# Performance work log

Measured on AMD Instinct MI355X. Metric: run time of the kernel, lower is better.

Reference implementation:

```python
import jax, jax.numpy as jnp
import numpy as np

B, S, E, R = 128, 16, 512, 1000
_SCALE = np.float32(1.0 / np.sqrt(E))


def setup_inputs() -> dict:
    key = jax.random.key(0)
    ks = jax.random.split(key, 12)
    s = 1.0 / np.sqrt(E)
    u = lambda k, shape: jax.random.uniform(k, shape, jnp.float32, -s, s)
    emb = jax.random.normal(ks[0], (R + 1, E), jnp.float32).at[R].set(0.0)  # padding_idx row = 0
    return {
        "tokens": jax.random.randint(ks[11], (B, S), 0, R),
        "emb": emb,
        "W_ih": u(ks[1], (3 * E, E)), "W_hh": u(ks[2], (3 * E, E)),
        "b_ih": u(ks[3], (3 * E,)), "b_hh": u(ks[4], (3 * E,)),
        "w_fc": u(ks[5], (E,)), "b_fc": u(ks[6], ()),
        "Wq": u(ks[7], (E, E)), "bq": u(ks[8], (E,)),
        "Wk": u(ks[9], (E, E)), "bk": u(ks[10], (E,)),
    }


def _gru_step(x, h, W_ih, W_hh, b_ih, b_hh):
    # torch GRU cell: gates stacked as [r; z; n]
    gi = x @ W_ih.T + b_ih
    gh = h @ W_hh.T + b_hh
    ir, iz, inn = jnp.split(gi, 3, axis=-1)
    hr, hz, hn = jnp.split(gh, 3, axis=-1)
    r = jax.nn.sigmoid(ir + hr)
    z = jax.nn.sigmoid(iz + hz)
    n = jnp.tanh(inn + r * hn)
    return (1.0 - z) * n + z * h


def _attention(x, emb, Wq, bq, Wk, bk):
    # x: [B,1,E]; key = fc_k(cat(relation_emb, x)); scores = q k^T / sqrt(E)
    Bn = x.shape[0]
    rel = jnp.broadcast_to(emb[:R][None], (Bn, R, E))
    all_emb = jnp.concatenate([rel, x], axis=1)        # [B,R+1,E]
    q = x @ Wq.T + bq
    k = all_emb @ Wk.T + bk
    scores = jnp.einsum('bqe,bke->bqk', q, k) * _SCALE  # [B,1,R+1]
    return scores, all_emb


def _entropy(scores):
    lp = jax.nn.log_softmax(scores, axis=-1)
    return -jnp.sum(jnp.exp(lp) * lp, axis=-1)          # [B,1]


def _reduce(x, emb, W_ih, W_hh, b_ih, b_hh, w_fc, b_fc, Wq, bq, Wk, bk):
    Bn, L, Ed = x.shape
    if L > 2:
        # vectorized 2-step GRU over all adjacent pairs (replaces python while loop)
        h1 = _gru_step(x[:, :-1], jnp.zeros_like(x[:, :-1]), W_ih, W_hh, b_ih, b_hh)
        pairs = _gru_step(x[:, 1:], h1, W_ih, W_hh, b_ih, b_hh)   # [B,L-1,E]
        score = jax.nn.sigmoid(pairs @ w_fc + b_fc)               # [B,L-1]
        sel = jnp.argmax(score, axis=-1)                          # [B]
        barange = jnp.arange(Bn)
        pair = pairs[barange, sel][:, None]                       # [B,1,E]
        scores, all_emb = _attention(pair, emb, Wq, bq, Wk, bk)
        loss = _entropy(scores)
        prob = jax.nn.softmax(scores, axis=-1)                    # weightedAverage mask is all-False for seq_len=1
        merged = jnp.einsum('bqk,bke->bqe', prob, all_emb)[:, 0]  # [B,E]
        # output = inputs.detach().clone(); overwrite sel with merged; delete row sel+1
        out = jax.lax.stop_gradient(x).at[barange, sel].set(merged)
        j = jnp.arange(L - 1)[None]
        src = j + (j >= (sel + 1)[:, None])                       # skip zeroed row sel+1
        out = out[barange[:, None], src]                          # [B,L-1,E]
        return out, loss
    else:
        h1 = _gru_step(x[:, 0], jnp.zeros_like(x[:, 0]), W_ih, W_hh, b_ih, b_hh)
        h2 = _gru_step(x[:, 1], h1, W_ih, W_hh, b_ih, b_hh)
        return h2[:, None], jnp.zeros((Bn, 1), x.dtype)


def reference(tokens, emb, W_ih, W_hh, b_ih, b_hh, w_fc, b_fc, Wq, bq, Wk, bk):
    x = emb[tokens]                                               # [B,S,E]
    losses = []
    for _ in range(tokens.shape[1] - 1):
        x, l = _reduce(x, emb, W_ih, W_hh, b_ih, b_hh, w_fc, b_fc, Wq, bq, Wk, bk)
        losses.append(l)
    scores, _ = _attention(x, emb, Wq, bq, Wk, bk)                # x is [B,1,E]
    losses.append(_entropy(scores))
    return scores[:, 0], jnp.concatenate(losses, axis=-1)         # ([B,R+1], [B,S])
```

## Files before the change

kernel.cpp:

```cpp
#include <hip/hip_runtime.h>

#define B 128
#define S 16
#define E 512
#define R 1000
#define K3 1536
#define NW0 1920
#define NWS 256
#define NS (B * (R + 1))
#define SCALE 0.04419417382415922f

static __device__ __forceinline__ float sigm(float x) { return 1.f / (1.f + expf(-x)); }

static __device__ __forceinline__ float brsum(float v, float* sb) {
  int tid = threadIdx.x;
  sb[tid] = v; __syncthreads();
  for (int s = 128; s > 0; s >>= 1) {
    if (tid < s) sb[tid] += sb[tid + s];
    __syncthreads();
  }
  float r = sb[0]; __syncthreads();
  return r;
}
static __device__ __forceinline__ float brmax(float v, float* sb) {
  int tid = threadIdx.x;
  sb[tid] = v; __syncthreads();
  for (int s = 128; s > 0; s >>= 1) {
    if (tid < s) sb[tid] = fmaxf(sb[tid], sb[tid + s]);
    __syncthreads();
  }
  float r = sb[0]; __syncthreads();
  return r;
}
static __device__ __forceinline__ void brsum2(float v1, float v2, float* sb, float* sb2,
                                              float* o1, float* o2) {
  int tid = threadIdx.x;
  sb[tid] = v1; sb2[tid] = v2; __syncthreads();
  for (int s = 128; s > 0; s >>= 1) {
    if (tid < s) { sb[tid] += sb[tid + s]; sb2[tid] += sb2[tid + s]; }
    __syncthreads();
  }
  *o1 = sb[0]; *o2 = sb2[0]; __syncthreads();
}

#define TILE_FMA \
  _Pragma("unroll") \
  for (int k = 0; k < 16; ++k) { \
    float4 a4 = *(const float4*)&As[k][ty * 4]; \
    float4 w4 = *(const float4*)&Ws[k][tx * 4]; \
    acc[0][0] = fmaf(a4.x, w4.x, acc[0][0]); acc[0][1] = fmaf(a4.x, w4.y, acc[0][1]); \
    acc[0][2] = fmaf(a4.x, w4.z, acc[0][2]); acc[0][3] = fmaf(a4.x, w4.w, acc[0][3]); \
    acc[1][0] = fmaf(a4.y, w4.x, acc[1][0]); acc[1][1] = fmaf(a4.y, w4.y, acc[1][1]); \
    acc[1][2] = fmaf(a4.y, w4.z, acc[1][2]); acc[1][3] = fmaf(a4.y, w4.w, acc[1][3]); \
    acc[2][0] = fmaf(a4.z, w4.x, acc[2][0]); acc[2][1] = fmaf(a4.z, w4.y, acc[2][1]); \
    acc[2][2] = fmaf(a4.z, w4.z, acc[2][2]); acc[2][3] = fmaf(a4.z, w4.w, acc[2][3]); \
    acc[3][0] = fmaf(a4.w, w4.x, acc[3][0]); acc[3][1] = fmaf(a4.w, w4.y, acc[3][1]); \
    acc[3][2] = fmaf(a4.w, w4.z, acc[3][2]); acc[3][3] = fmaf(a4.w, w4.w, acc[3][3]); \
  }

#define TILE_FMA32 \
  _Pragma("unroll") \
  for (int k = 0; k < 16; ++k) { \
    float2 a2 = *(const float2*)&As[k][ty * 2]; \
    float4 w4 = *(const float4*)&Ws[k][tx * 4]; \
    acc[0][0] = fmaf(a2.x, w4.x, acc[0][0]); acc[0][1] = fmaf(a2.x, w4.y, acc[0][1]); \
    acc[0][2] = fmaf(a2.x, w4.z, acc[0][2]); acc[0][3] = fmaf(a2.x, w4.w, acc[0][3]); \
    acc[1][0] = fmaf(a2.y, w4.x, acc[1][0]); acc[1][1] = fmaf(a2.y, w4.y, acc[1][1]); \
    acc[1][2] = fmaf(a2.y, w4.z, acc[1][2]); acc[1][3] = fmaf(a2.y, w4.w, acc[1][3]); \
  }

__global__ __launch_bounds__(256) void k_gemm(const float* __restrict__ A, int lda, int M,
                                              const float* __restrict__ W, int N, int K,
                                              const float* __restrict__ bias, float scale,
                                              float* __restrict__ C, int ldc) {
  __shared__ float As[16][64];
  __shared__ float Ws[16][64];
  int tid = threadIdx.x;
  int mBase = blockIdx.y * 64;
  int nBase = blockIdx.x * 64;
  int tx = tid & 15, ty = tid >> 4;
  int li = tid & 63;
  int lk = (tid >> 6) * 4;
  float acc[4][4] = {{0.f,0.f,0.f,0.f},{0.f,0.f,0.f,0.f},{0.f,0.f,0.f,0.f},{0.f,0.f,0.f,0.f}};
  int m = mBase + li;
  const float* Arow = (m < M) ? (A + (size_t)m * lda) : nullptr;
  int n = nBase + li;
  const float* Wrow = (n < N) ? (W + (size_t)n * K) : nullptr;

  float4 av = Arow ? *(const float4*)(Arow + lk) : make_float4(0.f, 0.f, 0.f, 0.f);
  float4 wv = Wrow ? *(const float4*)(Wrow + lk) : make_float4(0.f, 0.f, 0.f, 0.f);

  for (int k0 = 0; k0 < K; k0 += 16) {
    As[lk + 0][li] = av.x; As[lk + 1][li] = av.y;
    As[lk + 2][li] = av.z; As[lk + 3][li] = av.w;
    Ws[lk + 0][li] = wv.x; Ws[lk + 1][li] = wv.y;
    Ws[lk + 2][li] = wv.z; Ws[lk + 3][li] = wv.w;
    __syncthreads();
    if (k0 + 16 < K) {
      av = Arow ? *(const float4*)(Arow + k0 + 16 + lk) : make_float4(0.f, 0.f, 0.f, 0.f);
      wv = Wrow ? *(const float4*)(Wrow + k0 + 16 + lk) : make_float4(0.f, 0.f, 0.f, 0.f);
    }
    TILE_FMA
    __syncthreads();
  }
#pragma unroll
  for (int r = 0; r < 4; ++r) {
    int mm = mBase + ty * 4 + r;
    if (mm >= M) continue;
#pragma unroll
    for (int c = 0; c < 4; ++c) {
      int nn = nBase + tx * 4 + c;
      if (nn >= N) continue;
      float v = acc[r][c] * scale;
      if (bias) v += bias[nn];
      C[(size_t)mm * ldc + nn] = v;
    }
  }
}

__global__ __launch_bounds__(256) void k_gemmD(const float* __restrict__ A, int lda, int M,
                                               const float* __restrict__ W1, int N1,
                                               const float* __restrict__ b1,
                                               float* __restrict__ C1, int ldc1,
                                               const float* __restrict__ W2, int N2,
                                               float* __restrict__ C2, int ldc2, int K) {
  __shared__ float As[16][64];
  __shared__ float Ws[16][64];
  int tid = threadIdx.x;
  int mBase = blockIdx.y * 64;
  int nBase = blockIdx.x * 64;
  int tx = tid & 15, ty = tid >> 4;
  int li = tid & 63;
  int lk = (tid >> 6) * 4;
  float acc[4][4] = {{0.f,0.f,0.f,0.f},{0.f,0.f,0.f,0.f},{0.f,0.f,0.f,0.f},{0.f,0.f,0.f,0.f}};
  int m = mBase + li;
  const float* Arow = (m < M) ? (A + (size_t)m * lda) : nullptr;
  int n = nBase + li;
  const float* Wrow = nullptr;
  if (n < N1) Wrow = W1 + (size_t)n * K;
  else if (n < N1 + N2) Wrow = W2 + (size_t)(n - N1) * K;

  float4 av = Arow ? *(const float4*)(Arow + lk) : make_float4(0.f, 0.f, 0.f, 0.f);
  float4 wv = Wrow ? *(const float4*)(Wrow + lk) : make_float4(0.f, 0.f, 0.f, 0.f);

  for (int k0 = 0; k0 < K; k0 += 16) {
    As[lk + 0][li] = av.x; As[lk + 1][li] = av.y;
    As[lk + 2][li] = av.z; As[lk + 3][li] = av.w;
    Ws[lk + 0][li] = wv.x; Ws[lk + 1][li] = wv.y;
    Ws[lk + 2][li] = wv.z; Ws[lk + 3][li] = wv.w;
    __syncthreads();
    if (k0 + 16 < K) {
      av = Arow ? *(const float4*)(Arow + k0 + 16 + lk) : make_float4(0.f, 0.f, 0.f, 0.f);
      wv = Wrow ? *(const float4*)(Wrow + k0 + 16 + lk) : make_float4(0.f, 0.f, 0.f, 0.f);
    }
    TILE_FMA
    __syncthreads();
  }
#pragma unroll
  for (int r = 0; r < 4; ++r) {
    int mm = mBase + ty * 4 + r;
    if (mm >= M) continue;
#pragma unroll
    for (int c = 0; c < 4; ++c) {
      int nn = nBase + tx * 4 + c;
      if (nn < N1) {
        float v = acc[r][c];
        if (b1) v += b1[nn];
        C1[(size_t)mm * ldc1 + nn] = v;
      } else if (nn < N1 + N2) {
        C2[(size_t)mm * ldc2 + (nn - N1)] = acc[r][c];
      }
    }
  }
}

static __device__ void dev_g64(float (*As)[64], float (*Ws)[64], int tid,
                               int mBase, int nBase,
                               const float* __restrict__ A, int lda, int M,
                               const float* __restrict__ W, int N, int K,
                               const float* __restrict__ bias, float scale,
                               float* __restrict__ C, int ldc) {
  int tx = tid & 15, ty = tid >> 4;
  int li = tid & 63;
  int lk = (tid >> 6) * 4;
  float acc[4][4] = {{0.f,0.f,0.f,0.f},{0.f,0.f,0.f,0.f},{0.f,0.f,0.f,0.f},{0.f,0.f,0.f,0.f}};
  int m = mBase + li;
  const float* Arow = (m < M) ? (A + (size_t)m * lda) : nullptr;
  int n = nBase + li;
  const float* Wrow = (n < N) ? (W + (size_t)n * K) : nullptr;

  float4 av = Arow ? *(const float4*)(Arow + lk) : make_float4(0.f, 0.f, 0.f, 0.f);
  float4 wv = Wrow ? *(const float4*)(Wrow + lk) : make_float4(0.f, 0.f, 0.f, 0.f);

  for (int k0 = 0; k0 < K; k0 += 16) {
    As[lk + 0][li] = av.x; As[lk + 1][li] = av.y;
    As[lk + 2][li] = av.z; As[lk + 3][li] = av.w;
    Ws[lk + 0][li] = wv.x; Ws[lk + 1][li] = wv.y;
    Ws[lk + 2][li] = wv.z; Ws[lk + 3][li] = wv.w;
    __syncthreads();
    if (k0 + 16 < K) {
      av = Arow ? *(const float4*)(Arow + k0 + 16 + lk) : make_float4(0.f, 0.f, 0.f, 0.f);
      wv = Wrow ? *(const float4*)(Wrow + k0 + 16 + lk) : make_float4(0.f, 0.f, 0.f, 0.f);
    }
    TILE_FMA
    __syncthreads();
  }
#pragma unroll
  for (int r = 0; r < 4; ++r) {
    int mm = mBase + ty * 4 + r;
    if (mm >= M) continue;
#pragma unroll
    for (int c = 0; c < 4; ++c) {
      int nn = nBase + tx * 4 + c;
      if (nn >= N) continue;
      float v = acc[r][c] * scale;
      if (bias) v += bias[nn];
      C[(size_t)mm * ldc + nn] = v;
    }
  }
}

static __device__ void dev_tr64(float (*t)[65], int tid, const float* __restrict__ src,
                                int Cc, float* __restrict__ dst, int ldd, int bx, int by) {
  int tx = tid & 15, ty = tid >> 4;
  int rb = by * 64, cb = bx * 64;
#pragma unroll
  for (int i = 0; i < 4; ++i) {
    int r = rb + ty + i * 16;
    float4 v = *(const float4*)(src + (size_t)r * Cc + cb + tx * 4);
    t[ty + i * 16][tx * 4 + 0] = v.x; t[ty + i * 16][tx * 4 + 1] = v.y;
    t[ty + i * 16][tx * 4 + 2] = v.z; t[ty + i * 16][tx * 4 + 3] = v.w;
  }
  __syncthreads();
#pragma unroll
  for (int i = 0; i < 4; ++i) {
    int c = cb + ty + i * 16;
    float4 v;
    v.x = t[tx * 4 + 0][ty + i * 16]; v.y = t[tx * 4 + 1][ty + i * 16];
    v.z = t[tx * 4 + 2][ty + i * 16]; v.w = t[tx * 4 + 3][ty + i * 16];
    *(float4*)(dst + (size_t)c * ldd + rb + tx * 4) = v;
  }
}

__global__ __launch_bounds__(256) void k_prep(const float* __restrict__ Wq,
                                              const float* __restrict__ Wk,
                                              const float* __restrict__ Wih,
                                              float* __restrict__ WqT,
                                              float* __restrict__ WkT,
                                              float* __restrict__ Wbig,
                                              int* __restrict__ pos,
                                              int* __restrict__ wlb,
                                              int* __restrict__ wlL,
                                              int* __restrict__ wlR,
                                              float* __restrict__ outp) {
  __shared__ float t[64][65];
  int blk = blockIdx.x, tid = threadIdx.x;
  if (blk < 64) {
    dev_tr64(t, tid, Wq, E, WqT, E, blk & 7, blk >> 3);
  } else if (blk < 128) {
    int j = blk - 64;
    dev_tr64(t, tid, Wk, E, WkT, E, j & 7, j >> 3);
  } else if (blk < 320) {
    int j = blk - 128;
    dev_tr64(t, tid, Wih, E, Wbig + (size_t)1024 * K3, K3, j & 7, j >> 3);
  } else if (blk < 328) {
    int idx = (blk - 320) * 256 + tid;
    if (idx < B * 16) pos[idx] = idx & 15;
    if (idx < NW0) {
      wlb[idx] = idx / 15;
      int i = idx % 15;
      wlL[idx] = i;
      wlR[idx] = i + 1;
    }
    if (idx < B) outp[NS + idx * 16 + 14] = 0.f;
  } else {
    int idx = (blk - 328) * 256 + tid;
    for (int i = idx; i < 24 * K3; i += 8 * 256) Wbig[(size_t)1000 * K3 + i] = 0.f;
  }
}

__global__ __launch_bounds__(256) void k_setup3(const float* __restrict__ KREL,
                                                const float* __restrict__ WqT,
                                                const float* __restrict__ WkT,
                                                const float* __restrict__ bq,
                                                const float* __restrict__ bk,
                                                float* __restrict__ Gbig,
                                                float* __restrict__ v12,
                                                float* __restrict__ c0s,
                                                float* __restrict__ gb) {
  __shared__ float As[16][64];
  __shared__ float Ws[16][64];
  int blk = blockIdx.x, tid = threadIdx.x;
  if (blk < 128) {
    dev_g64(As, Ws, tid, (blk >> 3) * 64, (blk & 7) * 64, KREL, E, R, WqT, E, E,
            nullptr, 1.f, Gbig, E);
  } else if (blk < 192) {
    int j = blk - 128;
    dev_g64(As, Ws, tid, (j >> 3) * 64, (j & 7) * 64, WqT, E, E, WkT, E, E,
            nullptr, 1.f, Gbig + (size_t)1000 * E, E);
  } else {
    int m = blk - 192;
    if (m < 2) {
      int i = m * 256 + tid;
      const float* wq = WqT + (size_t)i * E;
      const float* wk = WkT + (size_t)i * E;
      float s = 0.f;
      for (int e = 0; e < E; ++e) s += wq[e] * bk[e] + bq[e] * wk[e];
      v12[i] = s;
    } else if (m == 2) {
      float* sb = (float*)As;
      float p = 0.f;
      for (int e = tid; e < E; e += 256) p += bq[e] * bk[e];
      float s = brsum(p, sb);
      if (tid == 0) c0s[0] = s;
    } else {
      int r = (m - 3) * 256 + tid;
      if (r < R) {
        const float* kr = KREL + (size_t)r * E;
        float s = 0.f;
        for (int e = 0; e < E; ++e) s += bq[e] * kr[e];
        gb[r] = s;
      }
    }
  }
}

__global__ __launch_bounds__(256) void k_giinit(const int* __restrict__ tokens,
                                                const float* __restrict__ Wbig,
                                                const float* __restrict__ bih,
                                                float* __restrict__ GI,
                                                const float* __restrict__ gb,
                                                float* __restrict__ SCT,
                                                const float* __restrict__ bhh,
                                                float* __restrict__ H1C) {
  int row = blockIdx.x, tid = threadIdx.x;
  if (row < B * S) {
    int tok = tokens[row];
    const float4* src = (const float4*)(Wbig + (size_t)tok * K3);
    const float4* bv = (const float4*)bih;
    float* girow = GI + (size_t)row * K3;
    float4* dst = (float4*)girow;
    for (int i = tid; i < K3 / 4; i += 256) {
      float4 a = src[i], b = bv[i];
      dst[i] = make_float4(a.x + b.x, a.y + b.y, a.z + b.z, a.w + b.w);
    }
    int i16 = row & 15;
    if (i16 < 15) {
      __syncthreads();
      float* h = H1C + (size_t)((row >> 4) * 15 + i16) * E;
      for (int e = tid; e < E; e += 256) {
        float r = sigm(girow[e] + bhh[e]);
        float z = sigm(girow[E + e] + bhh[E + e]);
        h[e] = (1.f - z) * tanhf(girow[2 * E + e] + r * bhh[2 * E + e]);
      }
    }
  } else {
    int rb = row - B * S;
    for (int m = rb * 16; m < rb * 16 + 16; ++m) {
      float* r = SCT + (size_t)m * K3;
      for (int n = tid; n < 1512; n += 256) r[n] = (n < 1000) ? gb[n] : 0.f;
    }
  }
}

__global__ __launch_bounds__(256) void k_h1c(const int* __restrict__ wlb,
                                             const int* __restrict__ wlL,
                                             const float* __restrict__ GI,
                                             const float* __restrict__ bhh,
                                             float* __restrict__ H1C,
                                             float* __restrict__ GHC) {
  int w = blockIdx.x, tid = threadIdx.x;
  const float* gi = GI + (size_t)(wlb[w] * 16 + wlL[w]) * K3;
  float* h = H1C + (size_t)w * E;
  for (int e = tid; e < E; e += 256) {
    float r = sigm(gi[e] + bhh[e]);
    float z = sigm(gi[E + e] + bhh[E + e]);
    h[e] = (1.f - z) * tanhf(gi[2 * E + e] + r * bhh[2 * E + e]);
  }
  if (GHC) {
    float* g = GHC + (size_t)w * K3;
    for (int n = tid; n < K3; n += 256) g[n] = bhh[n];
  }
}

__global__ __launch_bounds__(256) void k_ghcs(const float* __restrict__ H1C,
                                              const float* __restrict__ Whh,
                                              float* __restrict__ GHC) {
  __shared__ float As[16][32];
  __shared__ float Ws[16][64];
  int tid = threadIdx.x;
  int nBase = blockIdx.x * 64;
  int mBase = blockIdx.y * 32;
  int kbeg = blockIdx.z * 256;
  int tx = tid & 15, ty = tid >> 4;
  int ar = tid & 31, ak = (tid >> 5) * 2;
  int li = tid & 63, lk = (tid >> 6) * 4;
  float acc[2][4] = {{0.f,0.f,0.f,0.f},{0.f,0.f,0.f,0.f}};
  const float* Arow = H1C + (size_t)(mBase + ar) * E + kbeg;
  const float* Wrow = Whh + (size_t)(nBase + li) * E + kbeg;
  float2 av = *(const float2*)(Arow + ak);
  float4 wv = *(const float4*)(Wrow + lk);
  for (int k0 = 0; k0 < 256; k0 += 16) {
    As[ak + 0][ar] = av.x; As[ak + 1][ar] = av.y;
    Ws[lk + 0][li] = wv.x; Ws[lk + 1][li] = wv.y;
    Ws[lk + 2][li] = wv.z; Ws[lk + 3][li] = wv.w;
    __syncthreads();
    if (k0 + 16 < 256) {
      av = *(const float2*)(Arow + k0 + 16 + ak);
      wv = *(const float4*)(Wrow + k0 + 16 + lk);
    }
    TILE_FMA32
    __syncthreads();
  }
#pragma unroll
  for (int r = 0; r < 2; ++r) {
    int mm = mBase + ty * 2 + r;
#pragma unroll
    for (int c = 0; c < 4; ++c) {
      int nn = nBase + tx * 4 + c;
      atomicAdd(&GHC[(size_t)mm * K3 + nn], acc[r][c]);
    }
  }
}

__global__ __launch_bounds__(256) void k_pairc(const int* __restrict__ wlb,
                                               const int* __restrict__ wlL,
                                               const int* __restrict__ wlR,
                                               const float* __restrict__ GI,
                                               const float* __restrict__ GHC,
                                               const float* __restrict__ H1C,
                                               const float* __restrict__ wfc,
                                               const float* __restrict__ bfc,
                                               float* __restrict__ PAIR,
                                               float* __restrict__ SCR) {
  __shared__ float sb[256];
  int w = blockIdx.x, tid = threadIdx.x;
  int b = wlb[w], ls = wlL[w], rs = wlR[w];
  const float* gr = GI + (size_t)(b * 16 + rs) * K3;
  const float* gh = GHC + (size_t)w * K3;
  const float* h = H1C + (size_t)w * E;
  float* p = PAIR + (size_t)(b * 16 + ls) * E;
  float part = 0.f;
  for (int e = tid; e < E; e += 256) {
    float r = sigm(gr[e] + gh[e]);
    float z = sigm(gr[E + e] + gh[E + e]);
    float n = tanhf(gr[2 * E + e] + r * gh[2 * E + e]);
    float pv = (1.f - z) * n + z * h[e];
    p[e] = pv;
    part += pv * wfc[e];
  }
  float d = brsum(part, sb);
  if (tid == 0) SCR[b * 16 + ls] = sigm(d + bfc[0]);
}

__global__ __launch_bounds__(256) void k_qscsel(const float* __restrict__ PAIR,
                                                const float* __restrict__ SCR,
                                                const int* __restrict__ pin,
                                                int* __restrict__ pout,
                                                int* __restrict__ wlb,
                                                int* __restrict__ wlL,
                                                int* __restrict__ wlR,
                                                int* __restrict__ xdst,
                                                const float* __restrict__ Gbig,
                                                float* __restrict__ SCT,
                                                int P, int finalMode) {
  __shared__ float As[16][32];
  __shared__ float Ws[16][64];
  __shared__ int sxd[32];
  int tid = threadIdx.x;
  int nBase = blockIdx.x * 64;
  int mBase = blockIdx.y * 32;
  int kbeg = blockIdx.z * 256;
  if (tid < 32) {
    int b = mBase + tid;
    if (finalMode) {
      int xr = b * 16 + pin[b * 16];
      sxd[tid] = xr;
      if (blockIdx.x == 0 && blockIdx.z == 0) xdst[b] = xr;
    } else {
      int L = P + 1;
      int lp[16];
      for (int i = 0; i < L; ++i) lp[i] = pin[b * 16 + i];
      float best = -1e30f; int sel = 0;
      for (int i = 0; i < P; ++i) {
        float v = SCR[b * 16 + lp[i]];
        if (v > best) { best = v; sel = i; }
      }
      int r1i = (sel + 2 < L) ? sel + 2 : L - 1;
      int l1 = lp[sel], r1 = lp[r1i];
      int l0 = (sel > 0) ? lp[sel - 1] : l1;
      int r0 = (sel > 0) ? lp[sel] : r1;
      sxd[tid] = b * 16 + l1;
      if (blockIdx.x == 0 && blockIdx.z == 0) {
        wlb[2 * b] = b;     wlL[2 * b] = l0;     wlR[2 * b] = r0;
        wlb[2 * b + 1] = b; wlL[2 * b + 1] = l1; wlR[2 * b + 1] = r1;
        xdst[b] = b * 16 + l1;
        for (int i = 0; i < L - 1; ++i)
          pout[b * 16 + i] = (i <= sel) ? lp[i] : lp[i + 1];
      }
    }
  }
  __syncthreads();
  int tx = tid & 15, ty = tid >> 4;
  int ar = tid & 31, ak = (tid >> 5) * 2;
  int li = tid & 63, lk = (tid >> 6) * 4;
  float acc[2][4] = {{0.f,0.f,0.f,0.f},{0.f,0.f,0.f,0.f}};
  const float* Arow = PAIR + (size_t)sxd[ar] * E + kbeg;
  int n = nBase + li;
  const float* Wrow = (n < 1512) ? (Gbig + (size_t)n * E + kbeg) : nullptr;
  float2 av = *(const float2*)(Arow + ak);
  float4 wv = Wrow ? *(const float4*)(Wrow + lk) : make_float4(0.f, 0.f, 0.f, 0.f);
  for (int k0 = 0; k0 < 256; k0 += 16) {
    As[ak + 0][ar] = av.x; As[ak + 1][ar] = av.y;
    Ws[lk + 0][li] = wv.x; Ws[lk + 1][li] = wv.y;
    Ws[lk + 2][li] = wv.z; Ws[lk + 3][li] = wv.w;
    __syncthreads();
    if (k0 + 16 < 256) {
      av = *(const float2*)(Arow + k0 + 16 + ak);
      wv = Wrow ? *(const float4*)(Wrow + k0 + 16 + lk) : make_float4(0.f, 0.f, 0.f, 0.f);
    }
    TILE_FMA32
    __syncthreads();
  }
#pragma unroll
  for (int r = 0; r < 2; ++r) {
    int mm = mBase + ty * 2 + r;
#pragma unroll
    for (int c = 0; c < 4; ++c) {
      int nn = nBase + tx * 4 + c;
      if (nn < 1512) atomicAdd(&SCT[(size_t)mm * K3 + nn], acc[r][c]);
    }
  }
}

__global__ __launch_bounds__(256) void k_sm(float* __restrict__ SCT,
                                            const float* __restrict__ PAIR,
                                            const int* __restrict__ xdst,
                                            const float* __restrict__ v12,
                                            const float* __restrict__ c0s,
                                            float* __restrict__ outp,
                                            float* __restrict__ A2,
                                            float* __restrict__ GI,
                                            const float* __restrict__ bih,
                                            const float* __restrict__ gb,
                                            int t, int finalMode) {
  __shared__ float sb[256];
  __shared__ float sb2[256];
  __shared__ float sps[E];
  int b = blockIdx.x, tid = threadIdx.x;
  float* row = SCT + (size_t)b * K3;
  int xr = xdst[b];
  const float* sp = PAIR + (size_t)xr * E;
  for (int i = tid; i < E; i += 256) sps[i] = sp[i];
  __syncthreads();
  float part = 0.f;
  for (int i = tid; i < E; i += 256) part += sps[i] * (row[1000 + i] + v12[i]);
  float last = (brsum(part, sb) + c0s[0]) * SCALE;
  float s[4];
  float ml = last;
#pragma unroll
  for (int q = 0; q < 4; ++q) {
    int j = tid + q * 256;
    s[q] = (j < 1000) ? row[j] * SCALE : -1e30f;
    ml = fmaxf(ml, s[q]);
  }
  float mx = brmax(ml, sb);
  float zp = 0.f, s1p = 0.f;
#pragma unroll
  for (int q = 0; q < 4; ++q) {
    int j = tid + q * 256;
    if (j < 1000) { float e = expf(s[q] - mx); zp += e; s1p += e * s[q]; }
  }
  if (tid == 0) { float e = expf(last - mx); zp += e; s1p += e * last; }
  float z, s1;
  brsum2(zp, s1p, sb, sb2, &z, &s1);
  if (tid == 0) outp[NS + b * 16 + t] = mx + logf(z) - s1 / z;
  if (!finalMode) {
    float inv = 1.f / z;
    float* a = A2 + (size_t)b * K3;
#pragma unroll
    for (int q = 0; q < 4; ++q) {
      int j = tid + q * 256;
      if (j < 1000) a[j] = expf(s[q] - mx) * inv;
    }
    if (tid < 24) a[1000 + tid] = 0.f;
    float pr = expf(last - mx) * inv;
    for (int i = tid; i < E; i += 256) a[1024 + i] = pr * sps[i];
    float* g = GI + (size_t)xr * K3;
    for (int n2 = tid; n2 < K3; n2 += 256) g[n2] = bih[n2];
    for (int n2 = tid; n2 < 1512; n2 += 256) row[n2] = (n2 < 1000) ? gb[n2] : 0.f;
  } else {
    float* so = outp + (size_t)b * (R + 1);
#pragma unroll
    for (int q = 0; q < 4; ++q) {
      int j = tid + q * 256;
      if (j < 1000) so[j] = s[q];
    }
    if (tid == 0) so[R] = last;
  }
}

__global__ __launch_bounds__(256) void k_giup(const float* __restrict__ A2,
                                              const float* __restrict__ Wbig,
                                              float* __restrict__ GI,
                                              const int* __restrict__ xdst) {
  __shared__ float As[16][32];
  __shared__ float Ws[16][64];
  int tid = threadIdx.x;
  int nBase = blockIdx.x * 64;
  int mBase = blockIdx.y * 32;
  int kbeg = blockIdx.z * 384;
  int tx = tid & 15, ty = tid >> 4;
  int ar = tid & 31, ak = (tid >> 5) * 2;
  int li = tid & 63, wr = tid >> 6;
  float acc[2][4] = {{0.f,0.f,0.f,0.f},{0.f,0.f,0.f,0.f}};
  const float* Arow = A2 + (size_t)(mBase + ar) * K3;
  for (int k0 = kbeg; k0 < kbeg + 384; k0 += 16) {
    float2 av = *(const float2*)(Arow + k0 + ak);
    As[ak + 0][ar] = av.x; As[ak + 1][ar] = av.y;
#pragma unroll
    for (int j = 0; j < 4; ++j)
      Ws[wr * 4 + j][li] = Wbig[(size_t)(k0 + wr * 4 + j) * K3 + nBase + li];
    __syncthreads();
    TILE_FMA32
    __syncthreads();
  }
#pragma unroll
  for (int r = 0; r < 2; ++r) {
    int mm = mBase + ty * 2 + r;
    size_t crow = (size_t)xdst[mm] * K3;
#pragma unroll
    for (int c = 0; c < 4; ++c) {
      int nn = nBase + tx * 4 + c;
      atomicAdd(&GI[crow + nn], acc[r][c]);
    }
  }
}

extern "C" void kernel_launch(void* const* d_in, const int* in_sizes, int n_in,
                              void* d_out, int out_size, void* d_ws, size_t ws_size,
                              hipStream_t stream) {
  (void)in_sizes; (void)n_in; (void)out_size; (void)ws_size;
  const int* tokens = (const int*)d_in[0];
  const float* emb = (const float*)d_in[1];
  const float* W_ih = (const float*)d_in[2];
  const float* W_hh = (const float*)d_in[3];
  const float* b_ih = (const float*)d_in[4];
  const float* b_hh = (const float*)d_in[5];
  const float* w_fc = (const float*)d_in[6];
  const float* b_fc = (const float*)d_in[7];
  const float* Wq = (const float*)d_in[8];
  const float* bq = (const float*)d_in[9];
  const float* Wk = (const float*)d_in[10];
  const float* bk = (const float*)d_in[11];
  float* out = (float*)d_out;

  float* ws = (float*)d_ws;
  size_t o = 0;
  float* GI = ws + o;    o += (size_t)B * S * K3;
  float* GHC = ws + o;   o += (size_t)NW0 * K3;
  float* H1C = ws + o;   o += (size_t)NW0 * E;
  float* PAIR = ws + o;  o += (size_t)B * S * E;
  float* Wbig = ws + o;  o += (size_t)K3 * K3;
  float* Gbig = ws + o;  o += (size_t)1512 * E;
  float* KREL = ws + o;  o += (size_t)R * E;
  float* WqT = ws + o;   o += (size_t)E * E;
  float* WkT = ws + o;   o += (size_t)E * E;
  float* SCT = ws + o;   o += (size_t)B * K3;
  float* A2 = ws + o;    o += (size_t)B * K3;
  float* gb = ws + o;    o += 1024;
  float* v12 = ws + o;   o += 512;
  float* c0s = ws + o;   o += 16;
  float* SCR = ws + o;   o += B * 16;
  int* pos0 = (int*)(ws + o); o += B * 16;
  int* pos1 = (int*)(ws + o); o += B * 16;
  int* wlb = (int*)(ws + o);  o += NW0;
  int* wlL = (int*)(ws + o);  o += NW0;
  int* wlR = (int*)(ws + o);  o += NW0;
  int* xdst = (int*)(ws + o); o += B;

  k_prep<<<336, 256, 0, stream>>>(Wq, Wk, W_ih, WqT, WkT, Wbig, pos0, wlb, wlL, wlR, out);
  k_gemmD<<<dim3(32, 16), 256, 0, stream>>>(emb, E, R, Wk, E, bk, KREL, E,
                                            W_ih, K3, Wbig, K3, E);
  k_setup3<<<199, 256, 0, stream>>>(KREL, WqT, WkT, bq, bk, Gbig, v12, c0s, gb);
  k_giinit<<<B * S + 8, 256, 0, stream>>>(tokens, Wbig, b_ih, GI, gb, SCT, b_hh, H1C);
  k_gemm<<<dim3(24, 30), 256, 0, stream>>>(H1C, E, NW0, W_hh, K3, E, b_hh, 1.f, GHC, K3);
  k_pairc<<<NW0, 256, 0, stream>>>(wlb, wlL, wlR, GI, GHC, H1C, w_fc, b_fc, PAIR, SCR);

  for (int t = 0; t < 14; ++t) {
    int* pin = (t & 1) ? pos1 : pos0;
    int* pout = (t & 1) ? pos0 : pos1;
    k_qscsel<<<dim3(24, 4, 2), 256, 0, stream>>>(PAIR, SCR, pin, pout, wlb, wlL, wlR,
                                                 xdst, Gbig, SCT, 15 - t, 0);
    k_sm<<<B, 256, 0, stream>>>(SCT, PAIR, xdst, v12, c0s, out, A2, GI, b_ih, gb, t, 0);
    k_giup<<<dim3(24, 4, 4), 256, 0, stream>>>(A2, Wbig, GI, xdst);
    k_h1c<<<NWS, 256, 0, stream>>>(wlb, wlL, GI, b_hh, H1C, GHC);
    k_ghcs<<<dim3(24, 8, 2), 256, 0, stream>>>(H1C, W_hh, GHC);
    k_pairc<<<NWS, 256, 0, stream>>>(wlb, wlL, wlR, GI, GHC, H1C, w_fc, b_fc, PAIR, SCR);
  }

  k_qscsel<<<dim3(24, 4, 2), 256, 0, stream>>>(PAIR, SCR, pos0, pos1, wlb, wlL, wlR,
                                               xdst, Gbig, SCT, 1, 1);
  k_sm<<<B, 256, 0, stream>>>(SCT, PAIR, xdst, v12, c0s, out, A2, GI, b_ih, gb, 15, 1);
}
```

Before: 1.467 ms.

## Fuse GRU h1 computation into GHC split-K GEMM and shrink setup GEMM tiles

```diff
diff --git a/kernel.cpp b/kernel.cpp
--- a/kernel.cpp
+++ b/kernel.cpp
@@ -69,96 +69,90 @@
     acc[1][2] = fmaf(a2.y, w4.z, acc[1][2]); acc[1][3] = fmaf(a2.y, w4.w, acc[1][3]); \
   }
 
-__global__ __launch_bounds__(256) void k_gemm(const float* __restrict__ A, int lda, int M,
-                                              const float* __restrict__ W, int N, int K,
-                                              const float* __restrict__ bias, float scale,
-                                              float* __restrict__ C, int ldc) {
-  __shared__ float As[16][64];
+__global__ __launch_bounds__(256) void k_gemm32(const float* __restrict__ A, int lda, int M,
+                                                const float* __restrict__ W, int N, int K,
+                                                const float* __restrict__ bias,
+                                                float* __restrict__ C, int ldc) {
+  __shared__ float As[16][32];
   __shared__ float Ws[16][64];
   int tid = threadIdx.x;
-  int mBase = blockIdx.y * 64;
+  int mBase = blockIdx.y * 32;
   int nBase = blockIdx.x * 64;
   int tx = tid & 15, ty = tid >> 4;
-  int li = tid & 63;
-  int lk = (tid >> 6) * 4;
-  float acc[4][4] = {{0.f,0.f,0.f,0.f},{0.f,0.f,0.f,0.f},{0.f,0.f,0.f,0.f},{0.f,0.f,0.f,0.f}};
-  int m = mBase + li;
+  int ar = tid & 31, ak = (tid >> 5) * 2;
+  int li = tid & 63, lk = (tid >> 6) * 4;
+  float acc[2][4] = {{0.f,0.f,0.f,0.f},{0.f,0.f,0.f,0.f}};
+  int m = mBase + ar;
   const float* Arow = (m < M) ? (A + (size_t)m * lda) : nullptr;
   int n = nBase + li;
   const float* Wrow = (n < N) ? (W + (size_t)n * K) : nullptr;
-
-  float4 av = Arow ? *(const float4*)(Arow + lk) : make_float4(0.f, 0.f, 0.f, 0.f);
+  float2 av = Arow ? *(const float2*)(Arow + ak) : make_float2(0.f, 0.f);
   float4 wv = Wrow ? *(const float4*)(Wrow + lk) : make_float4(0.f, 0.f, 0.f, 0.f);
-
   for (int k0 = 0; k0 < K; k0 += 16) {
-    As[lk + 0][li] = av.x; As[lk + 1][li] = av.y;
-    As[lk + 2][li] = av.z; As[lk + 3][li] = av.w;
+    As[ak + 0][ar] = av.x; As[ak + 1][ar] = av.y;
     Ws[lk + 0][li] = wv.x; Ws[lk + 1][li] = wv.y;
     Ws[lk + 2][li] = wv.z; Ws[lk + 3][li] = wv.w;
     __syncthreads();
     if (k0 + 16 < K) {
-      av = Arow ? *(const float4*)(Arow + k0 + 16 + lk) : make_float4(0.f, 0.f, 0.f, 0.f);
+      av = Arow ? *(const float2*)(Arow + k0 + 16 + ak) : make_float2(0.f, 0.f);
       wv = Wrow ? *(const float4*)(Wrow + k0 + 16 + lk) : make_float4(0.f, 0.f, 0.f, 0.f);
     }
-    TILE_FMA
-    __syncthreads();
-  }
-#pragma unroll
-  for (int r = 0; r < 4; ++r) {
-    int mm = mBase + ty * 4 + r;
+    TILE_FMA32
+    __syncthreads();
+  }
+#pragma unroll
+  for (int r = 0; r < 2; ++r) {
+    int mm = mBase + ty * 2 + r;
     if (mm >= M) continue;
 #pragma unroll
     for (int c = 0; c < 4; ++c) {
       int nn = nBase + tx * 4 + c;
       if (nn >= N) continue;
-      float v = acc[r][c] * scale;
+      float v = acc[r][c];
       if (bias) v += bias[nn];
       C[(size_t)mm * ldc + nn] = v;
     }
   }
 }
 
-__global__ __launch_bounds__(256) void k_gemmD(const float* __restrict__ A, int lda, int M,
-                                               const float* __restrict__ W1, int N1,
-                                               const float* __restrict__ b1,
-                                               float* __restrict__ C1, int ldc1,
-                                               const float* __restrict__ W2, int N2,
-                                               float* __restrict__ C2, int ldc2, int K) {
-  __shared__ float As[16][64];
+__global__ __launch_bounds__(256) void k_gemmD32(const float* __restrict__ A, int lda, int M,
+                                                 const float* __restrict__ W1, int N1,
+                                                 const float* __restrict__ b1,
+                                                 float* __restrict__ C1, int ldc1,
+                                                 const float* __restrict__ W2, int N2,
+                                                 float* __restrict__ C2, int ldc2, int K) {
+  __shared__ float As[16][32];
   __shared__ float Ws[16][64];
   int tid = threadIdx.x;
-  int mBase = blockIdx.y * 64;
+  int mBase = blockIdx.y * 32;
   int nBase = blockIdx.x * 64;
   int tx = tid & 15, ty = tid >> 4;
-  int li = tid & 63;
-  int lk = (tid >> 6) * 4;
-  float acc[4][4] = {{0.f,0.f,0.f,0.f},{0.f,0.f,0.f,0.f},{0.f,0.f,0.f,0.f},{0.f,0.f,0.f,0.f}};
-  int m = mBase + li;
+  int ar = tid & 31, ak = (tid >> 5) * 2;
+  int li = tid & 63, lk = (tid >> 6) * 4;
+  float acc[2][4] = {{0.f,0.f,0.f,0.f},{0.f,0.f,0.f,0.f}};
+  int m = mBase + ar;
   const float* Arow = (m < M) ? (A + (size_t)m * lda) : nullptr;
   int n = nBase + li;
   const float* Wrow = nullptr;
   if (n < N1) Wrow = W1 + (size_t)n * K;
   else if (n < N1 + N2) Wrow = W2 + (size_t)(n - N1) * K;
-
-  float4 av = Arow ? *(const float4*)(Arow + lk) : make_float4(0.f, 0.f, 0.f, 0.f);
+  float2 av = Arow ? *(const float2*)(Arow + ak) : make_float2(0.f, 0.f);
   float4 wv = Wrow ? *(const float4*)(Wrow + lk) : make_float4(0.f, 0.f, 0.f, 0.f);
-
   for (int k0 = 0; k0 < K; k0 += 16) {
-    As[lk + 0][li] = av.x; As[lk + 1][li] = av.y;
-    As[lk + 2][li] = av.z; As[lk + 3][li] = av.w;
+    As[ak + 0][ar] = av.x; As[ak + 1][ar] = av.y;
     Ws[lk + 0][li] = wv.x; Ws[lk + 1][li] = wv.y;
     Ws[lk + 2][li] = wv.z; Ws[lk + 3][li] = wv.w;
     __syncthreads();
     if (k0 + 16 < K) {
-      av = Arow ? *(const float4*)(Arow + k0 + 16 + lk) : make_float4(0.f, 0.f, 0.f, 0.f);
+      av = Arow ? *(const float2*)(Arow + k0 + 16 + ak) : make_float2(0.f, 0.f);
       wv = Wrow ? *(const float4*)(Wrow + k0 + 16 + lk) : make_float4(0.f, 0.f, 0.f, 0.f);
     }
-    TILE_FMA
-    __syncthreads();
-  }
-#pragma unroll
-  for (int r = 0; r < 4; ++r) {
-    int mm = mBase + ty * 4 + r;
+    TILE_FMA32
+    __syncthreads();
+  }
+#pragma unroll
+  for (int r = 0; r < 2; ++r) {
+    int mm = mBase + ty * 2 + r;
     if (mm >= M) continue;
 #pragma unroll
     for (int c = 0; c < 4; ++c) {
@@ -363,29 +357,13 @@
   }
 }
 
-__global__ __launch_bounds__(256) void k_h1c(const int* __restrict__ wlb,
-                                             const int* __restrict__ wlL,
-                                             const float* __restrict__ GI,
-                                             const float* __restrict__ bhh,
-                                             float* __restrict__ H1C,
-                                             float* __restrict__ GHC) {
-  int w = blockIdx.x, tid = threadIdx.x;
-  const float* gi = GI + (size_t)(wlb[w] * 16 + wlL[w]) * K3;
-  float* h = H1C + (size_t)w * E;
-  for (int e = tid; e < E; e += 256) {
-    float r = sigm(gi[e] + bhh[e]);
-    float z = sigm(gi[E + e] + bhh[E + e]);
-    h[e] = (1.f - z) * tanhf(gi[2 * E + e] + r * bhh[2 * E + e]);
-  }
-  if (GHC) {
-    float* g = GHC + (size_t)w * K3;
-    for (int n = tid; n < K3; n += 256) g[n] = bhh[n];
-  }
-}
-
-__global__ __launch_bounds__(256) void k_ghcs(const float* __restrict__ H1C,
+__global__ __launch_bounds__(256) void k_ghcs(const int* __restrict__ wlb,
+                                              const int* __restrict__ wlL,
+                                              const float* __restrict__ GI,
+                                              const float* __restrict__ bhh,
                                               const float* __restrict__ Whh,
-                                              float* __restrict__ GHC) {
+                                              float* __restrict__ GHC,
+                                              float* __restrict__ H1C) {
   __shared__ float As[16][32];
   __shared__ float Ws[16][64];
   int tid = threadIdx.x;
@@ -395,18 +373,38 @@
   int tx = tid & 15, ty = tid >> 4;
   int ar = tid & 31, ak = (tid >> 5) * 2;
   int li = tid & 63, lk = (tid >> 6) * 4;
+  int w = mBase + ar;
+  const float* gi = GI + (size_t)(wlb[w] * 16 + wlL[w]) * K3;
+  const float* Wrow = Whh + (size_t)(nBase + li) * E + kbeg;
+  int writeH = (blockIdx.x == 0);
+  float* hrow = H1C + (size_t)w * E;
   float acc[2][4] = {{0.f,0.f,0.f,0.f},{0.f,0.f,0.f,0.f}};
-  const float* Arow = H1C + (size_t)(mBase + ar) * E + kbeg;
-  const float* Wrow = Whh + (size_t)(nBase + li) * E + kbeg;
-  float2 av = *(const float2*)(Arow + ak);
+  int e0 = kbeg + ak;
+  float2 g0 = *(const float2*)(gi + e0);
+  float2 g1 = *(const float2*)(gi + E + e0);
+  float2 g2 = *(const float2*)(gi + 2 * E + e0);
+  float2 b0 = *(const float2*)(bhh + e0);
+  float2 b1 = *(const float2*)(bhh + E + e0);
+  float2 b2 = *(const float2*)(bhh + 2 * E + e0);
   float4 wv = *(const float4*)(Wrow + lk);
   for (int k0 = 0; k0 < 256; k0 += 16) {
-    As[ak + 0][ar] = av.x; As[ak + 1][ar] = av.y;
+    float r0 = sigm(g0.x + b0.x), z0 = sigm(g1.x + b1.x);
+    float h0 = (1.f - z0) * tanhf(g2.x + r0 * b2.x);
+    float r1 = sigm(g0.y + b0.y), z1 = sigm(g1.y + b1.y);
+    float h1v = (1.f - z1) * tanhf(g2.y + r1 * b2.y);
+    As[ak + 0][ar] = h0; As[ak + 1][ar] = h1v;
     Ws[lk + 0][li] = wv.x; Ws[lk + 1][li] = wv.y;
     Ws[lk + 2][li] = wv.z; Ws[lk + 3][li] = wv.w;
+    if (writeH) *(float2*)(hrow + kbeg + k0 + ak) = make_float2(h0, h1v);
     __syncthreads();
     if (k0 + 16 < 256) {
-      av = *(const float2*)(Arow + k0 + 16 + ak);
+      int e2 = kbeg + k0 + 16 + ak;
+      g0 = *(const float2*)(gi + e2);
+      g1 = *(const float2*)(gi + E + e2);
+      g2 = *(const float2*)(gi + 2 * E + e2);
+      b0 = *(const float2*)(bhh + e2);
+      b1 = *(const float2*)(bhh + E + e2);
+      b2 = *(const float2*)(bhh + 2 * E + e2);
       wv = *(const float4*)(Wrow + k0 + 16 + lk);
     }
     TILE_FMA32
@@ -543,6 +541,8 @@
                                             float* __restrict__ GI,
                                             const float* __restrict__ bih,
                                             const float* __restrict__ gb,
+                                            float* __restrict__ GHC,
+                                            const float* __restrict__ bhh,
                                             int t, int finalMode) {
   __shared__ float sb[256];
   __shared__ float sb2[256];
@@ -589,6 +589,12 @@
     float* g = GI + (size_t)xr * K3;
     for (int n2 = tid; n2 < K3; n2 += 256) g[n2] = bih[n2];
     for (int n2 = tid; n2 < 1512; n2 += 256) row[n2] = (n2 < 1000) ? gb[n2] : 0.f;
+    float* g0 = GHC + (size_t)(2 * b) * K3;
+    float* g1 = GHC + (size_t)(2 * b + 1) * K3;
+    for (int n2 = tid; n2 < K3; n2 += 256) {
+      float bb = bhh[n2];
+      g0[n2] = bb; g1[n2] = bb;
+    }
   } else {
     float* so = outp + (size_t)b * (R + 1);
 #pragma unroll
@@ -680,11 +686,11 @@
   int* xdst = (int*)(ws + o); o += B;
 
   k_prep<<<336, 256, 0, stream>>>(Wq, Wk, W_ih, WqT, WkT, Wbig, pos0, wlb, wlL, wlR, out);
-  k_gemmD<<<dim3(32, 16), 256, 0, stream>>>(emb, E, R, Wk, E, bk, KREL, E,
-                                            W_ih, K3, Wbig, K3, E);
+  k_gemmD32<<<dim3(32, 32), 256, 0, stream>>>(emb, E, R, Wk, E, bk, KREL, E,
+                                              W_ih, K3, Wbig, K3, E);
   k_setup3<<<199, 256, 0, stream>>>(KREL, WqT, WkT, bq, bk, Gbig, v12, c0s, gb);
   k_giinit<<<B * S + 8, 256, 0, stream>>>(tokens, Wbig, b_ih, GI, gb, SCT, b_hh, H1C);
-  k_gemm<<<dim3(24, 30), 256, 0, stream>>>(H1C, E, NW0, W_hh, K3, E, b_hh, 1.f, GHC, K3);
+  k_gemm32<<<dim3(24, 60), 256, 0, stream>>>(H1C, E, NW0, W_hh, K3, E, b_hh, GHC, K3);
   k_pairc<<<NW0, 256, 0, stream>>>(wlb, wlL, wlR, GI, GHC, H1C, w_fc, b_fc, PAIR, SCR);
 
   for (int t = 0; t < 14; ++t) {
@@ -692,14 +698,15 @@
     int* pout = (t & 1) ? pos0 : pos1;
     k_qscsel<<<dim3(24, 4, 2), 256, 0, stream>>>(PAIR, SCR, pin, pout, wlb, wlL, wlR,
                                                  xdst, Gbig, SCT, 15 - t, 0);
-    k_sm<<<B, 256, 0, stream>>>(SCT, PAIR, xdst, v12, c0s, out, A2, GI, b_ih, gb, t, 0);
+    k_sm<<<B, 256, 0, stream>>>(SCT, PAIR, xdst, v12, c0s, out, A2, GI, b_ih, gb,
+                                GHC, b_hh, t, 0);
     k_giup<<<dim3(24, 4, 4), 256, 0, stream>>>(A2, Wbig, GI, xdst);
-    k_h1c<<<NWS, 256, 0, stream>>>(wlb, wlL, GI, b_hh, H1C, GHC);
-    k_ghcs<<<dim3(24, 8, 2), 256, 0, stream>>>(H1C, W_hh, GHC);
+    k_ghcs<<<dim3(24, 8, 2), 256, 0, stream>>>(wlb, wlL, GI, b_hh, W_hh, GHC, H1C);
     k_pairc<<<NWS, 256, 0, stream>>>(wlb, wlL, wlR, GI, GHC, H1C, w_fc, b_fc, PAIR, SCR);
   }
 
   k_qscsel<<<dim3(24, 4, 2), 256, 0, stream>>>(PAIR, SCR, pos0, pos1, wlb, wlL, wlR,
                                                xdst, Gbig, SCT, 1, 1);
-  k_sm<<<B, 256, 0, stream>>>(SCT, PAIR, xdst, v12, c0s, out, A2, GI, b_ih, gb, 15, 1);
-}
+  k_sm<<<B, 256, 0, stream>>>(SCT, PAIR, xdst, v12, c0s, out, A2, GI, b_ih, gb,
+                              GHC, b_hh, 15, 1);
+}
```

Result: slower. 1.600 ms (+9.1%).
